# Optimization experiments

Measured on AMD Instinct MI355X. Metric: run time of the kernel, lower is better.

Reference implementation:

```python
import jax, jax.numpy as jnp
import numpy as np

PAD = 1  # PAD_token; embedding rows at PAD are zero (padding_idx)


def setup_inputs() -> dict:
    V, D, HOPS = 50000, 128, 3
    B, Lc, Mc = 16, 256, 8
    Lk, Mk = 512, 8
    key = jax.random.key(0)
    kC, kK, kc, kk = jax.random.split(key, 4)
    # one table per hop (C_0..C_{HOPS-1}, K_0..K_{HOPS-1}), init N(0, 0.1)
    C = 0.1 * jax.random.normal(kC, (HOPS, V, D), dtype=jnp.float32)
    K = 0.1 * jax.random.normal(kK, (HOPS, V, D), dtype=jnp.float32)
    C = C.at[:, PAD].set(0.0)
    K = K.at[:, PAD].set(0.0)
    conv_seqs = jax.random.randint(kc, (B, Lc, Mc), 0, V)
    kb_arr = jax.random.randint(kk, (B, Lk, Mk), 0, V)  # dense, PAD-padded ragged KB
    return {"conv_seqs": conv_seqs, "kb_arr": kb_arr, "C": C, "K": K}


def reference(conv_seqs, kb_arr, C, K):
    B, Lc, _ = conv_seqs.shape
    HOPS, _, D = C.shape
    conv_feature = jnp.zeros((B, Lc, D), dtype=C.dtype)
    for hop in range(HOPS):
        # embedding-bag: gather + sum over span tokens
        cf = jnp.sum(C[hop][conv_seqs], axis=2)  # [B, Lc, D]
        kf = jnp.sum(K[hop][kb_arr], axis=2)     # [B, Lk, D]
        att = jnp.einsum('bld,bkd->blk', cf, kf)  # [B, Lc, Lk]
        p = jax.nn.softmax(att, axis=-1)
        conv_feature = jnp.einsum('blk,bkd->bld', p, kf) + conv_feature
    return conv_feature.transpose(1, 0, 2)  # [Lc, B, D]
```

## Files before the change

kernel.cpp:

```cpp
#include <hip/hip_runtime.h>

#define V_    50000
#define D_    128
#define HOPS_ 3
#define B_    16
#define LC_   256
#define MC_   8
#define LK_   512
#define MK_   8

typedef __bf16  bf16x8  __attribute__((ext_vector_type(8)));
typedef unsigned short ushort8 __attribute__((ext_vector_type(8)));
typedef float   floatx4 __attribute__((ext_vector_type(4)));

__device__ inline unsigned short f2bf(float f) {
    union { float f; unsigned u; } x; x.f = f;
    unsigned r = x.u + 0x7FFFu + ((x.u >> 16) & 1u);
    return (unsigned short)(r >> 16);
}

__device__ inline floatx4 mfma_bf16(ushort8 a, ushort8 b, floatx4 c) {
    return __builtin_amdgcn_mfma_f32_16x16x32_bf16(
        __builtin_bit_cast(bf16x8, a), __builtin_bit_cast(bf16x8, b), c, 0, 0, 0);
}

__global__ __launch_bounds__(256) void gather_kernel(
    const int* __restrict__ conv_seqs, const int* __restrict__ kb_arr,
    const float* __restrict__ Ct, const float* __restrict__ Kt,
    unsigned short* __restrict__ kf, unsigned short* __restrict__ kfT,
    unsigned short* __restrict__ cf, float4* __restrict__ out4)
{
    __shared__ float tile[32][132];

    const int tid  = threadIdx.x;
    const int bx   = blockIdx.x;

    constexpr int KBLK = HOPS_ * B_ * (LK_ / 32);
    constexpr int CBLK = HOPS_ * B_ * (LC_ / 32);

    if (bx >= KBLK + CBLK) {
        int zb = bx - (KBLK + CBLK);
        out4[(size_t)zb * 256 + tid] = make_float4(0.f, 0.f, 0.f, 0.f);
        return;
    }

    const int r    = tid >> 3;
    const int s    = tid & 7;
    const int d0   = s * 16;
    const int lane = tid & 63;

    const int*   idxp;
    const float* table;
    unsigned short* dst;
    bool do_transpose;
    int hop, b, row0;

    if (bx < KBLK) {
        hop  = bx / (B_ * 16);
        int rem = bx % (B_ * 16);
        b    = rem >> 4;
        row0 = (rem & 15) * 32;
        idxp  = kb_arr + (size_t)(b * LK_ + row0 + r) * MK_;
        table = Kt + (size_t)hop * V_ * D_;
        dst   = kf + (((size_t)(hop * B_ + b) * LK_) + row0 + r) * D_ + d0;
        do_transpose = true;
    } else {
        int id = bx - KBLK;
        hop  = id / (B_ * 8);
        int rem = id % (B_ * 8);
        b    = rem >> 3;
        row0 = (rem & 7) * 32;
        idxp  = conv_seqs + (size_t)(b * LC_ + row0 + r) * MC_;
        table = Ct + (size_t)hop * V_ * D_;
        dst   = cf + (((size_t)(hop * B_ + b) * LC_) + row0 + r) * D_ + d0;
        do_transpose = false;
    }

    const int myidx = idxp[s];

    float4 acc[4];
    #pragma unroll
    for (int j = 0; j < 4; ++j) acc[j] = make_float4(0.f, 0.f, 0.f, 0.f);

    #pragma unroll
    for (int m = 0; m < 8; ++m) {
        int idx = __shfl(myidx, (lane & 56) + m);
        const float4* src = (const float4*)(table + (size_t)idx * D_ + d0);
        #pragma unroll
        for (int j = 0; j < 4; ++j) {
            float4 v = src[j];
            acc[j].x += v.x; acc[j].y += v.y; acc[j].z += v.z; acc[j].w += v.w;
        }
    }

    {
        ushort8 o0, o1;
        o0[0] = f2bf(acc[0].x); o0[1] = f2bf(acc[0].y);
        o0[2] = f2bf(acc[0].z); o0[3] = f2bf(acc[0].w);
        o0[4] = f2bf(acc[1].x); o0[5] = f2bf(acc[1].y);
        o0[6] = f2bf(acc[1].z); o0[7] = f2bf(acc[1].w);
        o1[0] = f2bf(acc[2].x); o1[1] = f2bf(acc[2].y);
        o1[2] = f2bf(acc[2].z); o1[3] = f2bf(acc[2].w);
        o1[4] = f2bf(acc[3].x); o1[5] = f2bf(acc[3].y);
        o1[6] = f2bf(acc[3].z); o1[7] = f2bf(acc[3].w);
        *(ushort8*)(dst)     = o0;
        *(ushort8*)(dst + 8) = o1;
    }

    if (do_transpose) {
        #pragma unroll
        for (int j = 0; j < 4; ++j)
            *(float4*)&tile[r][d0 + j * 4] = acc[j];
        __syncthreads();
        const int d    = tid >> 1;
        const int koff = (tid & 1) * 16;
        unsigned short* tdst =
            kfT + ((size_t)(hop * B_ + b) * D_ + d) * LK_ + row0 + koff;
        #pragma unroll
        for (int i0 = 0; i0 < 16; i0 += 8) {
            ushort8 o;
            #pragma unroll
            for (int i = 0; i < 8; ++i) o[i] = f2bf(tile[koff + i0 + i][d]);
            *(ushort8*)(tdst + i0) = o;
        }
    }
}

__global__ __launch_bounds__(512) void attn_kernel(
    const unsigned short* __restrict__ kf, const unsigned short* __restrict__ kfT,
    const unsigned short* __restrict__ cf, float* __restrict__ out)
{
    constexpr int AS = 516;
    __shared__ float att_s[16][AS];
    __shared__ float rowinv_s[16];

    const int tid  = threadIdx.x;
    const int wave = tid >> 6;
    const int lane = tid & 63;
    const int quad = lane >> 4;
    const int l16  = lane & 15;

    const int gl  = blockIdx.x & 7;
    const int s_  = blockIdx.x >> 3;
    const int lt  = s_ / 6;
    const int gh  = s_ % 6;
    const int g   = gh * 8 + gl;
    const int hop = g >> 4;
    const int b   = g & 15;
    const int l0  = lt * 16;

    const unsigned short* cf_h  = cf  + (((size_t)g) * 256 + l0) * 128;
    const unsigned short* kf_h  = kf  + ((size_t)g) * 512 * 128;
    const unsigned short* kfT_h = kfT + ((size_t)g) * 128 * 512;

    ushort8 afrag[4];
    #pragma unroll
    for (int ks = 0; ks < 4; ++ks)
        afrag[ks] = *(const ushort8*)(cf_h + l16 * 128 + ks * 32 + quad * 8);

    #pragma unroll
    for (int t = 0; t < 4; ++t) {
        const int nt = wave * 4 + t;
        floatx4 acc = {0.f, 0.f, 0.f, 0.f};
        #pragma unroll
        for (int ks = 0; ks < 4; ++ks) {
            ushort8 bfrag = *(const ushort8*)(kf_h + (nt * 16 + l16) * 128 + ks * 32 + quad * 8);
            acc = mfma_bf16(afrag[ks], bfrag, acc);
        }
        #pragma unroll
        for (int rr = 0; rr < 4; ++rr)
            att_s[quad * 4 + rr][nt * 16 + l16] = acc[rr];
    }
    __syncthreads();

    #pragma unroll
    for (int rr = 0; rr < 2; ++rr) {
        const int row = wave * 2 + rr;
        float v[8];
        float mx = -1e30f;
        #pragma unroll
        for (int j = 0; j < 8; ++j) {
            v[j] = att_s[row][lane + j * 64];
            mx = fmaxf(mx, v[j]);
        }
        #pragma unroll
        for (int off = 32; off; off >>= 1) mx = fmaxf(mx, __shfl_xor(mx, off));
        float sum = 0.f;
        #pragma unroll
        for (int j = 0; j < 8; ++j) {
            float e = __expf(v[j] - mx);
            att_s[row][lane + j * 64] = e;
            sum += e;
        }
        #pragma unroll
        for (int off = 32; off; off >>= 1) sum += __shfl_xor(sum, off);
        if (lane == 0) rowinv_s[row] = 1.0f / sum;
    }
    __syncthreads();

    floatx4 pacc = {0.f, 0.f, 0.f, 0.f};
    #pragma unroll
    for (int ks = 0; ks < 16; ++ks) {
        const float* prow = &att_s[l16][ks * 32 + quad * 8];
        float4 p0 = *(const float4*)(prow);
        float4 p1 = *(const float4*)(prow + 4);
        ushort8 pa;
        pa[0] = f2bf(p0.x); pa[1] = f2bf(p0.y); pa[2] = f2bf(p0.z); pa[3] = f2bf(p0.w);
        pa[4] = f2bf(p1.x); pa[5] = f2bf(p1.y); pa[6] = f2bf(p1.z); pa[7] = f2bf(p1.w);
        ushort8 bfrag = *(const ushort8*)(kfT_h + (size_t)(wave * 16 + l16) * 512 + ks * 32 + quad * 8);
        pacc = mfma_bf16(pa, bfrag, pacc);
    }

    const int d = wave * 16 + l16;
    #pragma unroll
    for (int rr = 0; rr < 4; ++rr)
        atomicAdd(&out[(((size_t)(l0 + quad * 4 + rr)) * 16 + b) * 128 + d],
                  pacc[rr] * rowinv_s[quad * 4 + rr]);
}

extern "C" void kernel_launch(void* const* d_in, const int* in_sizes, int n_in,
                              void* d_out, int out_size, void* d_ws, size_t ws_size,
                              hipStream_t stream) {
    (void)in_sizes; (void)n_in; (void)out_size; (void)ws_size;
    const int*   conv_seqs = (const int*)d_in[0];
    const int*   kb_arr    = (const int*)d_in[1];
    const float* C         = (const float*)d_in[2];
    const float* K         = (const float*)d_in[3];

    unsigned short* kf  = (unsigned short*)d_ws;
    unsigned short* kfT = kf  + (size_t)HOPS_ * B_ * LK_ * D_;
    unsigned short* cf  = kfT + (size_t)HOPS_ * B_ * LK_ * D_;
    float* out = (float*)d_out;

    hipLaunchKernelGGL(gather_kernel, dim3(1664), dim3(256), 0, stream,
                       conv_seqs, kb_arr, C, K, kf, kfT, cf, (float4*)out);
    hipLaunchKernelGGL(attn_kernel, dim3(768), dim3(512), 0, stream,
                       kf, kfT, cf, out);
}
```

Baseline: 196.0 us.

## Split kf transpose into separate kernel and coalesce gather row reads

Gather no longer transposes kf in shared memory. Each 8-thread group now reads an embedding row as interleaved float4 chunks, so consecutive lanes touch contiguous addresses. A new bf16 transpose kernel builds kfT from kf and also zeroes the output, which frees the gather kernel of LDS and syncs and allows a higher occupancy hint. This adds a third kernel launch and an extra global read and write of kf.

```diff
diff --git a/kernel.cpp b/kernel.cpp
--- a/kernel.cpp
+++ b/kernel.cpp
@@ -11,6 +11,7 @@
 
 typedef __bf16  bf16x8  __attribute__((ext_vector_type(8)));
 typedef unsigned short ushort8 __attribute__((ext_vector_type(8)));
+typedef unsigned short ushort4v __attribute__((ext_vector_type(4)));
 typedef float   floatx4 __attribute__((ext_vector_type(4)));
 
 __device__ inline unsigned short f2bf(float f) {
@@ -24,59 +25,47 @@
         __builtin_bit_cast(bf16x8, a), __builtin_bit_cast(bf16x8, b), c, 0, 0, 0);
 }
 
-__global__ __launch_bounds__(256) void gather_kernel(
+__global__ __launch_bounds__(256, 7) void gather_kernel(
     const int* __restrict__ conv_seqs, const int* __restrict__ kb_arr,
     const float* __restrict__ Ct, const float* __restrict__ Kt,
-    unsigned short* __restrict__ kf, unsigned short* __restrict__ kfT,
-    unsigned short* __restrict__ cf, float4* __restrict__ out4)
+    unsigned short* __restrict__ kf, unsigned short* __restrict__ cf)
 {
-    __shared__ float tile[32][132];
-
     const int tid  = threadIdx.x;
-    const int bx   = blockIdx.x;
-
-    constexpr int KBLK = HOPS_ * B_ * (LK_ / 32);
-    constexpr int CBLK = HOPS_ * B_ * (LC_ / 32);
-
-    if (bx >= KBLK + CBLK) {
-        int zb = bx - (KBLK + CBLK);
-        out4[(size_t)zb * 256 + tid] = make_float4(0.f, 0.f, 0.f, 0.f);
-        return;
-    }
-
     const int r    = tid >> 3;
     const int s    = tid & 7;
-    const int d0   = s * 16;
     const int lane = tid & 63;
+    const int bx   = blockIdx.x;
+
+    constexpr int KBLK = HOPS_ * B_ * (LK_ / 32);
 
     const int*   idxp;
     const float* table;
     unsigned short* dst;
-    bool do_transpose;
-    int hop, b, row0;
 
     if (bx < KBLK) {
-        hop  = bx / (B_ * 16);
-        int rem = bx % (B_ * 16);
-        b    = rem >> 4;
-        row0 = (rem & 15) * 32;
+        int hop  = bx / (B_ * 16);
+        int rem  = bx % (B_ * 16);
+        int b    = rem >> 4;
+        int row0 = (rem & 15) * 32;
         idxp  = kb_arr + (size_t)(b * LK_ + row0 + r) * MK_;
         table = Kt + (size_t)hop * V_ * D_;
-        dst   = kf + (((size_t)(hop * B_ + b) * LK_) + row0 + r) * D_ + d0;
-        do_transpose = true;
+        dst   = kf + (((size_t)(hop * B_ + b) * LK_) + row0 + r) * D_;
     } else {
-        int id = bx - KBLK;
-        hop  = id / (B_ * 8);
-        int rem = id % (B_ * 8);
-        b    = rem >> 3;
-        row0 = (rem & 7) * 32;
+        int id   = bx - KBLK;
+        int hop  = id / (B_ * 8);
+        int rem  = id % (B_ * 8);
+        int b    = rem >> 3;
+        int row0 = (rem & 7) * 32;
         idxp  = conv_seqs + (size_t)(b * LC_ + row0 + r) * MC_;
         table = Ct + (size_t)hop * V_ * D_;
-        dst   = cf + (((size_t)(hop * B_ + b) * LC_) + row0 + r) * D_ + d0;
-        do_transpose = false;
+        dst   = cf + (((size_t)(hop * B_ + b) * LC_) + row0 + r) * D_;
     }
 
     const int myidx = idxp[s];
+    int idxs[8];
+    #pragma unroll
+    for (int m = 0; m < 8; ++m)
+        idxs[m] = __shfl(myidx, (lane & 56) + m);
 
     float4 acc[4];
     #pragma unroll
@@ -84,46 +73,60 @@
 
     #pragma unroll
     for (int m = 0; m < 8; ++m) {
-        int idx = __shfl(myidx, (lane & 56) + m);
-        const float4* src = (const float4*)(table + (size_t)idx * D_ + d0);
+        const float* rowp = table + (size_t)idxs[m] * D_;
         #pragma unroll
         for (int j = 0; j < 4; ++j) {
-            float4 v = src[j];
+            float4 v = *(const float4*)(rowp + j * 32 + s * 4);
             acc[j].x += v.x; acc[j].y += v.y; acc[j].z += v.z; acc[j].w += v.w;
         }
     }
 
-    {
-        ushort8 o0, o1;
-        o0[0] = f2bf(acc[0].x); o0[1] = f2bf(acc[0].y);
-        o0[2] = f2bf(acc[0].z); o0[3] = f2bf(acc[0].w);
-        o0[4] = f2bf(acc[1].x); o0[5] = f2bf(acc[1].y);
-        o0[6] = f2bf(acc[1].z); o0[7] = f2bf(acc[1].w);
-        o1[0] = f2bf(acc[2].x); o1[1] = f2bf(acc[2].y);
-        o1[2] = f2bf(acc[2].z); o1[3] = f2bf(acc[2].w);
-        o1[4] = f2bf(acc[3].x); o1[5] = f2bf(acc[3].y);
-        o1[6] = f2bf(acc[3].z); o1[7] = f2bf(acc[3].w);
-        *(ushort8*)(dst)     = o0;
-        *(ushort8*)(dst + 8) = o1;
-    }
-
-    if (do_transpose) {
-        #pragma unroll
-        for (int j = 0; j < 4; ++j)
-            *(float4*)&tile[r][d0 + j * 4] = acc[j];
-        __syncthreads();
-        const int d    = tid >> 1;
-        const int koff = (tid & 1) * 16;
-        unsigned short* tdst =
-            kfT + ((size_t)(hop * B_ + b) * D_ + d) * LK_ + row0 + koff;
-        #pragma unroll
-        for (int i0 = 0; i0 < 16; i0 += 8) {
-            ushort8 o;
-            #pragma unroll
-            for (int i = 0; i < 8; ++i) o[i] = f2bf(tile[koff + i0 + i][d]);
-            *(ushort8*)(tdst + i0) = o;
-        }
-    }
+    #pragma unroll
+    for (int j = 0; j < 4; ++j) {
+        ushort4v o;
+        o[0] = f2bf(acc[j].x); o[1] = f2bf(acc[j].y);
+        o[2] = f2bf(acc[j].z); o[3] = f2bf(acc[j].w);
+        *(ushort4v*)(dst + j * 32 + s * 4) = o;
+    }
+}
+
+__global__ __launch_bounds__(256) void transpose_kernel(
+    const unsigned short* __restrict__ kf, unsigned short* __restrict__ kfT,
+    float4* __restrict__ out4)
+{
+    __shared__ unsigned short tile[64][72];
+
+    const int tid = threadIdx.x;
+    const int bx  = blockIdx.x;
+
+    if (bx >= 768) {
+        out4[(size_t)(bx - 768) * 256 + tid] = make_float4(0.f, 0.f, 0.f, 0.f);
+        return;
+    }
+
+    const int g  = bx >> 4;
+    const int dt = (bx & 15) >> 3;
+    const int kt = bx & 7;
+    const int k0 = kt * 64, d0 = dt * 64;
+
+    const int r = tid >> 2;
+    const int c = tid & 3;
+
+    const unsigned short* src = kf + ((size_t)g * 512 + k0 + r) * 128 + d0 + c * 16;
+    ushort8 a = *(const ushort8*)(src);
+    ushort8 b = *(const ushort8*)(src + 8);
+    *(ushort8*)&tile[r][c * 16]     = a;
+    *(ushort8*)&tile[r][c * 16 + 8] = b;
+    __syncthreads();
+
+    unsigned short* dstp = kfT + ((size_t)g * 128 + d0 + r) * 512 + k0 + c * 16;
+    ushort8 o0, o1;
+    #pragma unroll
+    for (int i = 0; i < 8; ++i) o0[i] = tile[c * 16 + i][r];
+    #pragma unroll
+    for (int i = 0; i < 8; ++i) o1[i] = tile[c * 16 + 8 + i][r];
+    *(ushort8*)(dstp)     = o0;
+    *(ushort8*)(dstp + 8) = o1;
 }
 
 __global__ __launch_bounds__(512) void attn_kernel(
@@ -145,7 +148,6 @@
     const int lt  = s_ / 6;
     const int gh  = s_ % 6;
     const int g   = gh * 8 + gl;
-    const int hop = g >> 4;
     const int b   = g & 15;
     const int l0  = lt * 16;
 
@@ -232,8 +234,10 @@
     unsigned short* cf  = kfT + (size_t)HOPS_ * B_ * LK_ * D_;
     float* out = (float*)d_out;
 
-    hipLaunchKernelGGL(gather_kernel, dim3(1664), dim3(256), 0, stream,
-                       conv_seqs, kb_arr, C, K, kf, kfT, cf, (float4*)out);
+    hipLaunchKernelGGL(gather_kernel, dim3(1152), dim3(256), 0, stream,
+                       conv_seqs, kb_arr, C, K, kf, cf);
+    hipLaunchKernelGGL(transpose_kernel, dim3(1280), dim3(256), 0, stream,
+                       kf, kfT, (float4*)out);
     hipLaunchKernelGGL(attn_kernel, dim3(768), dim3(512), 0, stream,
                        kf, kfT, cf, out);
 }
```

New measurement: 194.2 us. No clear change (-0.9%).
